# Optimization experiments

Measured on AMD Instinct MI355X. Metric: run time of the kernel, lower is better.

## Reference

```python
import jax, jax.numpy as jnp
import numpy as np

N, F, H, E, G, C = 100000, 128, 128, 640000, 512, 6
EPS = 1e-5


def setup_inputs() -> dict:
    key = jax.random.key(0)
    ks = jax.random.split(key, 20)
    def w(k, shape, fan_in):
        return jax.random.normal(k, shape, jnp.float32) * (1.0 / np.sqrt(fan_in))
    return {
        "x": jax.random.normal(ks[0], (N, F), jnp.float32),
        "edge_index": jax.random.randint(ks[1], (2, E), 0, N),
        "batch": jnp.sort(jax.random.randint(ks[2], (N,), 0, G)),
        "num_graphs": G,
        # SAGEConv1: lin_l (aggregated, with bias) + lin_r (root, no bias)
        "W1l": w(ks[3], (F, H), F), "b1l": jnp.zeros((H,), jnp.float32), "W1r": w(ks[4], (F, H), F),
        # SAGEConv2
        "W2l": w(ks[5], (H, H), H), "b2l": jnp.zeros((H,), jnp.float32), "W2r": w(ks[6], (H, H), H),
        # cluster heads
        "Wc1": w(ks[7], (H, H), H), "bc1": jnp.zeros((H,), jnp.float32),
        "Wc2": w(ks[8], (H, 2), H), "bc2": jnp.zeros((2,), jnp.float32),
        # classifier
        "Wl1": w(ks[9], (H, H), H), "bl1": jnp.zeros((H,), jnp.float32),
        "Wl2": w(ks[10], (H, C), H), "bl2": jnp.zeros((C,), jnp.float32),
    }


def _sage(x, src, dst, Wl, bl, Wr):
    # PyG SAGEConv: mean-aggregate messages x[src] at dst, then lin_l(agg) + lin_r(x)
    n = x.shape[0]
    s = jax.ops.segment_sum(x[src], dst, num_segments=n)
    cnt = jax.ops.segment_sum(jnp.ones((src.shape[0],), x.dtype), dst, num_segments=n)
    agg = s / jnp.maximum(cnt, 1.0)[:, None]
    return agg @ Wl + bl + x @ Wr


def reference(x, edge_index, batch, num_graphs,
              W1l, b1l, W1r, W2l, b2l, W2r,
              Wc1, bc1, Wc2, bc2, Wl1, bl1, Wl2, bl2):
    src, dst = edge_index[0], edge_index[1]
    h = jax.nn.relu(_sage(x, src, dst, W1l, b1l, W1r))
    h = jax.nn.relu(_sage(h, src, dst, W2l, b2l, W2r))
    # 2-way soft cluster assignment per node
    a = jax.nn.softmax(jnp.tanh(h @ Wc1 + bc1) @ Wc2 + bc2, axis=1)  # [N,2]
    g = num_graphs
    # group_features[g] = a_g^T h_g  -> per-node outer product, segment-summed by graph
    gf = jax.ops.segment_sum(a[:, :, None] * h[:, None, :], batch, num_segments=g)  # [G,2,H]
    pos = gf[:, 0, :]  # positive-cluster embedding per graph
    # new_adj[g] = a_g^T A_g a_g ; only within-graph edges appear in the per-graph adj block
    same = (batch[src] == batch[dst]).astype(h.dtype)
    contrib = same[:, None, None] * (a[src][:, :, None] * a[dst][:, None, :])  # [E,2,2]
    new_adj = jax.ops.segment_sum(contrib, batch[src], num_segments=g)  # [G,2,2]
    # F.normalize(p=1, dim=1, eps=1e-5): row-wise L1 with clamped denominator
    l1 = jnp.sum(jnp.abs(new_adj), axis=2, keepdims=True)
    norm_adj = new_adj / jnp.maximum(l1, EPS)
    diag = jnp.diagonal(norm_adj, axis1=1, axis2=2)  # [G,2]
    penalty = jnp.mean(jnp.mean((diag - 1.0) ** 2, axis=1))  # mse vs ones(2), averaged over graphs
    # NOTE: original (faithfully reproduced) takes the mean over ALL nodes, same for every graph
    graph_emb = jnp.broadcast_to(jnp.mean(h, axis=0, keepdims=True), (g, h.shape[1]))
    z = jax.nn.relu(pos @ Wl1 + bl1)  # dropout off (eval mode)
    logits = z @ Wl2 + bl2
    return (jax.nn.log_softmax(logits, axis=-1), pos, graph_emb, penalty)
```

## Files before the change

kernel.cpp:

```cpp
#include <hip/hip_runtime.h>

#define NN 100000
#define NE 640000
#define HD 128
#define NG 512
#define NC 6
#define EPSV 1e-5f
#define OCT 12500

typedef __bf16 bf16_t;
typedef bf16_t bf16x8 __attribute__((ext_vector_type(8)));
typedef float f32x4 __attribute__((ext_vector_type(4)));

__device__ __forceinline__ float b2f(unsigned int u16) {
    return __builtin_bit_cast(float, u16 << 16);
}
__device__ __forceinline__ unsigned short f2b(float f) {
    unsigned int u = __builtin_bit_cast(unsigned int, f);
    unsigned int r = (u + 0x7fffu + ((u >> 16) & 1u)) >> 16;
    return (unsigned short)r;
}

__global__ __launch_bounds__(256) void k_zero(uint4* __restrict__ p, int n16) {
    int i = blockIdx.x * 256 + threadIdx.x;
    if (i < n16) p[i] = (uint4){0u, 0u, 0u, 0u};
}

__global__ __launch_bounds__(256) void k_prep(
    const float* __restrict__ x, unsigned short* __restrict__ xb,
    const float* __restrict__ Wa, const float* __restrict__ Wb,
    const float* __restrict__ Wc, const float* __restrict__ Wd,
    const float* __restrict__ We, unsigned short* __restrict__ Wt,
    const int* __restrict__ dst, int* __restrict__ cnt)
{
    int bid = blockIdx.x;
    if (bid < 960) {
        int oct = bid & 7;
        int widx = bid >> 3;
        int lo = oct * OCT, hi = lo + OCT;
        for (int e = widx * 256 + threadIdx.x; e < NE; e += 120 * 256) {
            int d = dst[e];
            if (d >= lo && d < hi) atomicAdd(&cnt[d], 1);
        }
    } else if (bid < 7210) {
        int i = (bid - 960) * 256 + threadIdx.x;
        float4 v0 = reinterpret_cast<const float4*>(x)[i * 2];
        float4 v1 = reinterpret_cast<const float4*>(x)[i * 2 + 1];
        unsigned short u[8] = {f2b(v0.x), f2b(v0.y), f2b(v0.z), f2b(v0.w),
                               f2b(v1.x), f2b(v1.y), f2b(v1.z), f2b(v1.w)};
        reinterpret_cast<uint4*>(xb)[i] = *reinterpret_cast<uint4*>(u);
    } else {
        int i = (bid - 7210) * 256 + threadIdx.x;
        int w = i >> 14, r = i & 16383;
        int k = r >> 7, n = r & 127;
        const float* W = (w == 0) ? Wa : (w == 1) ? Wb : (w == 2) ? Wc : (w == 3) ? Wd : We;
        Wt[w * 16384 + n * HD + k] = f2b(W[k * HD + n]);
    }
}

__global__ void k_scan1(const int* __restrict__ cnt, int* __restrict__ excl,
                        int* __restrict__ bsum, int n) {
    __shared__ int sh[256];
    int i = blockIdx.x * 256 + threadIdx.x;
    int v = (i < n) ? cnt[i] : 0;
    sh[threadIdx.x] = v;
    __syncthreads();
    for (int off = 1; off < 256; off <<= 1) {
        int t = (threadIdx.x >= off) ? sh[threadIdx.x - off] : 0;
        __syncthreads();
        sh[threadIdx.x] += t;
        __syncthreads();
    }
    if (i < n) excl[i] = sh[threadIdx.x] - v;
    if (threadIdx.x == 255) bsum[blockIdx.x] = sh[255];
}

__global__ void k_scan2(int* bsum, int nb) {
    __shared__ int sh[512];
    int t = threadIdx.x;
    sh[t] = (t < nb) ? bsum[t] : 0;
    __syncthreads();
    for (int off = 1; off < 512; off <<= 1) {
        int v = (t >= off) ? sh[t - off] : 0;
        __syncthreads();
        sh[t] += v;
        __syncthreads();
    }
    if (t < nb) bsum[t] = sh[t];
}

__global__ void k_scan3(const int* __restrict__ excl, const int* __restrict__ bsum,
                        int* __restrict__ row_off, int n) {
    int i = blockIdx.x * 256 + threadIdx.x;
    if (i < n) row_off[i] = excl[i] + (blockIdx.x ? bsum[blockIdx.x - 1] : 0);
    if (i == 0) row_off[n] = NE;
}

__global__ __launch_bounds__(256) void k_fill(const int* __restrict__ src,
                                              const int* __restrict__ dst,
                                              const int* __restrict__ row_off,
                                              int* __restrict__ cnt,
                                              int* __restrict__ csr) {
    int q = blockIdx.x;
    int oct = q & 7;
    int widx = q >> 3;
    int lo = oct * OCT, hi = lo + OCT;
    for (int e = widx * 256 + threadIdx.x; e < NE; e += 120 * 256) {
        int d = dst[e];
        if (d >= lo && d < hi) {
            int p = atomicSub(&cnt[d], 1);
            csr[row_off[d] + p - 1] = src[e];
        }
    }
}

__global__ __launch_bounds__(256) void k_sage(
    const unsigned short* __restrict__ X,
    const int* __restrict__ row_off, const int* __restrict__ csr,
    const unsigned short* __restrict__ Wlt, const unsigned short* __restrict__ Wrt,
    const float* __restrict__ bias, unsigned short* __restrict__ out, int M)
{
    __shared__ uint4 wlds[4096];
    const int wid = threadIdx.x >> 6;
    const int lane = threadIdx.x & 63;
    const int lrow = lane & 15;
    const int lkg = lane >> 4;
    const int r0 = blockIdx.x * 64 + wid * 16;

    const uint4* gl = reinterpret_cast<const uint4*>(Wlt);
    const uint4* gr = reinterpret_cast<const uint4*>(Wrt);
    for (int i = threadIdx.x; i < 2048; i += 256) {
        int di = i ^ ((i >> 4) & 7);
        wlds[di] = gl[i];
        wlds[2048 + di] = gr[i];
    }

    int row = r0 + lrow;
    row = row < M ? row : M - 1;
    int beg = row_off[row], end = row_off[row + 1];

    float accg[4][8];
#pragma unroll
    for (int ks = 0; ks < 4; ++ks)
#pragma unroll
        for (int j = 0; j < 8; ++j) accg[ks][j] = 0.f;

    const unsigned short* Xk = X + lkg * 8;
    for (int j = beg; j < end; j += 2) {
        int s0 = csr[j];
        const unsigned short* p0 = Xk + (size_t)s0 * HD;
        uint4 w0 = *reinterpret_cast<const uint4*>(p0);
        uint4 w1 = *reinterpret_cast<const uint4*>(p0 + 32);
        uint4 w2 = *reinterpret_cast<const uint4*>(p0 + 64);
        uint4 w3 = *reinterpret_cast<const uint4*>(p0 + 96);
        bool ok1 = (j + 1) < end;
        int s1 = csr[ok1 ? j + 1 : j];
        const unsigned short* p1 = Xk + (size_t)s1 * HD;
        uint4 y0, y1, y2, y3;
        if (ok1) {
            y0 = *reinterpret_cast<const uint4*>(p1);
            y1 = *reinterpret_cast<const uint4*>(p1 + 32);
            y2 = *reinterpret_cast<const uint4*>(p1 + 64);
            y3 = *reinterpret_cast<const uint4*>(p1 + 96);
        }
        accg[0][0] += b2f(w0.x & 0xffffu); accg[0][1] += b2f(w0.x >> 16);
        accg[0][2] += b2f(w0.y & 0xffffu); accg[0][3] += b2f(w0.y >> 16);
        accg[0][4] += b2f(w0.z & 0xffffu); accg[0][5] += b2f(w0.z >> 16);
        accg[0][6] += b2f(w0.w & 0xffffu); accg[0][7] += b2f(w0.w >> 16);
        accg[1][0] += b2f(w1.x & 0xffffu); accg[1][1] += b2f(w1.x >> 16);
        accg[1][2] += b2f(w1.y & 0xffffu); accg[1][3] += b2f(w1.y >> 16);
        accg[1][4] += b2f(w1.z & 0xffffu); accg[1][5] += b2f(w1.z >> 16);
        accg[1][6] += b2f(w1.w & 0xffffu); accg[1][7] += b2f(w1.w >> 16);
        accg[2][0] += b2f(w2.x & 0xffffu); accg[2][1] += b2f(w2.x >> 16);
        accg[2][2] += b2f(w2.y & 0xffffu); accg[2][3] += b2f(w2.y >> 16);
        accg[2][4] += b2f(w2.z & 0xffffu); accg[2][5] += b2f(w2.z >> 16);
        accg[2][6] += b2f(w2.w & 0xffffu); accg[2][7] += b2f(w2.w >> 16);
        accg[3][0] += b2f(w3.x & 0xffffu); accg[3][1] += b2f(w3.x >> 16);
        accg[3][2] += b2f(w3.y & 0xffffu); accg[3][3] += b2f(w3.y >> 16);
        accg[3][4] += b2f(w3.z & 0xffffu); accg[3][5] += b2f(w3.z >> 16);
        accg[3][6] += b2f(w3.w & 0xffffu); accg[3][7] += b2f(w3.w >> 16);
        if (ok1) {
            accg[0][0] += b2f(y0.x & 0xffffu); accg[0][1] += b2f(y0.x >> 16);
            accg[0][2] += b2f(y0.y & 0xffffu); accg[0][3] += b2f(y0.y >> 16);
            accg[0][4] += b2f(y0.z & 0xffffu); accg[0][5] += b2f(y0.z >> 16);
            accg[0][6] += b2f(y0.w & 0xffffu); accg[0][7] += b2f(y0.w >> 16);
            accg[1][0] += b2f(y1.x & 0xffffu); accg[1][1] += b2f(y1.x >> 16);
            accg[1][2] += b2f(y1.y & 0xffffu); accg[1][3] += b2f(y1.y >> 16);
            accg[1][4] += b2f(y1.z & 0xffffu); accg[1][5] += b2f(y1.z >> 16);
            accg[1][6] += b2f(y1.w & 0xffffu); accg[1][7] += b2f(y1.w >> 16);
            accg[2][0] += b2f(y2.x & 0xffffu); accg[2][1] += b2f(y2.x >> 16);
            accg[2][2] += b2f(y2.y & 0xffffu); accg[2][3] += b2f(y2.y >> 16);
            accg[2][4] += b2f(y2.z & 0xffffu); accg[2][5] += b2f(y2.z >> 16);
            accg[2][6] += b2f(y2.w & 0xffffu); accg[2][7] += b2f(y2.w >> 16);
            accg[3][0] += b2f(y3.x & 0xffffu); accg[3][1] += b2f(y3.x >> 16);
            accg[3][2] += b2f(y3.y & 0xffffu); accg[3][3] += b2f(y3.y >> 16);
            accg[3][4] += b2f(y3.z & 0xffffu); accg[3][5] += b2f(y3.z >> 16);
            accg[3][6] += b2f(y3.w & 0xffffu); accg[3][7] += b2f(y3.w >> 16);
        }
    }

    float inv = 1.f / fmaxf((float)(end - beg), 1.f);
    bf16x8 a1[4], a2f[4];
#pragma unroll
    for (int ks = 0; ks < 4; ++ks) {
        unsigned short u[8];
#pragma unroll
        for (int j = 0; j < 8; ++j) u[j] = f2b(accg[ks][j] * inv);
        a1[ks] = *reinterpret_cast<bf16x8*>(u);
    }
    const unsigned short* p2 = X + (size_t)row * HD + lkg * 8;
#pragma unroll
    for (int ks = 0; ks < 4; ++ks)
        a2f[ks] = *reinterpret_cast<const bf16x8*>(p2 + ks * 32);

    f32x4 acc[8];
#pragma unroll
    for (int t = 0; t < 8; ++t) {
        float b = bias[t * 16 + lrow];
        acc[t] = (f32x4){b, b, b, b};
    }

    __syncthreads();

    const char* ldsb = (const char*)wlds;
#pragma unroll
    for (int ks = 0; ks < 4; ++ks) {
#pragma unroll
        for (int t = 0; t < 8; ++t) {
            int off = (lrow * 256 + lkg * 16 + t * 4096 + ks * 64) ^ ((lrow & 7) << 4);
            bf16x8 bl = *reinterpret_cast<const bf16x8*>(ldsb + off);
            bf16x8 br = *reinterpret_cast<const bf16x8*>(ldsb + 32768 + off);
            acc[t] = __builtin_amdgcn_mfma_f32_16x16x32_bf16(a1[ks], bl, acc[t], 0, 0, 0);
            acc[t] = __builtin_amdgcn_mfma_f32_16x16x32_bf16(a2f[ks], br, acc[t], 0, 0, 0);
        }
    }

#pragma unroll
    for (int t = 0; t < 8; ++t)
#pragma unroll
        for (int r = 0; r < 4; ++r) {
            int orow = r0 + lkg * 4 + r;
            if (orow < M)
                out[(size_t)orow * HD + t * 16 + lrow] = f2b(fmaxf(acc[t][r], 0.f));
        }
}

__global__ __launch_bounds__(256) void mfma_attn(
    const unsigned short* __restrict__ A1, const unsigned short* __restrict__ W1t,
    const float* __restrict__ bias, const float* __restrict__ Wc2,
    const float* __restrict__ bc2, float* __restrict__ a2, int M)
{
    __shared__ uint4 wlds[2048];
    const int wid = threadIdx.x >> 6;
    const int lane = threadIdx.x & 63;
    const int lrow = lane & 15;
    const int lkg = lane >> 4;
    const int r0 = blockIdx.x * 128 + wid * 32;

    bf16x8 a[2][4];
#pragma unroll
    for (int g = 0; g < 2; ++g) {
        int row = r0 + g * 16 + lrow;
        row = row < M ? row : M - 1;
        const unsigned short* p = A1 + (size_t)row * HD + lkg * 8;
#pragma unroll
        for (int ks = 0; ks < 4; ++ks)
            a[g][ks] = *reinterpret_cast<const bf16x8*>(p + ks * 32);
    }

    f32x4 acc[2][8];
#pragma unroll
    for (int t = 0; t < 8; ++t) {
        float b = bias[t * 16 + lrow];
        acc[0][t] = (f32x4){b, b, b, b};
        acc[1][t] = (f32x4){b, b, b, b};
    }

    const uint4* g4 = reinterpret_cast<const uint4*>(W1t);
    for (int i = threadIdx.x; i < 2048; i += 256) {
        int di = i ^ ((i >> 4) & 7);
        wlds[di] = g4[i];
    }
    __syncthreads();

    const char* ldsb = (const char*)wlds;
#pragma unroll
    for (int ks = 0; ks < 4; ++ks) {
#pragma unroll
        for (int t = 0; t < 8; ++t) {
            int off = (lrow * 256 + lkg * 16 + t * 4096 + ks * 64) ^ ((lrow & 7) << 4);
            bf16x8 b = *reinterpret_cast<const bf16x8*>(ldsb + off);
            acc[0][t] = __builtin_amdgcn_mfma_f32_16x16x32_bf16(a[0][ks], b, acc[0][t], 0, 0, 0);
            acc[1][t] = __builtin_amdgcn_mfma_f32_16x16x32_bf16(a[1][ks], b, acc[1][t], 0, 0, 0);
        }
    }

    float p0[2][4] = {{0.f, 0.f, 0.f, 0.f}, {0.f, 0.f, 0.f, 0.f}};
    float p1[2][4] = {{0.f, 0.f, 0.f, 0.f}, {0.f, 0.f, 0.f, 0.f}};
#pragma unroll
    for (int t = 0; t < 8; ++t) {
        float2 wv = reinterpret_cast<const float2*>(Wc2)[t * 16 + lrow];
#pragma unroll
        for (int g = 0; g < 2; ++g)
#pragma unroll
            for (int r = 0; r < 4; ++r) {
                float tv = tanhf(acc[g][t][r]);
                p0[g][r] = fmaf(tv, wv.x, p0[g][r]);
                p1[g][r] = fmaf(tv, wv.y, p1[g][r]);
            }
    }
#pragma unroll
    for (int off = 1; off < 16; off <<= 1) {
#pragma unroll
        for (int g = 0; g < 2; ++g)
#pragma unroll
            for (int r = 0; r < 4; ++r) {
                p0[g][r] += __shfl_xor(p0[g][r], off, 64);
                p1[g][r] += __shfl_xor(p1[g][r], off, 64);
            }
    }
    if (lrow == 0) {
        float B0 = bc2[0], B1 = bc2[1];
#pragma unroll
        for (int g = 0; g < 2; ++g)
#pragma unroll
            for (int r = 0; r < 4; ++r) {
                int row = r0 + g * 16 + lkg * 4 + r;
                if (row < M) {
                    float u0 = p0[g][r] + B0, u1 = p1[g][r] + B1;
                    float m = fmaxf(u0, u1);
                    float e0 = expf(u0 - m), e1 = expf(u1 - m);
                    float inv = 1.f / (e0 + e1);
                    reinterpret_cast<float2*>(a2)[row] = (float2){e0 * inv, e1 * inv};
                }
            }
    }
}

__global__ __launch_bounds__(1024) void k_posadj(const unsigned short* __restrict__ h,
                                                 const float* __restrict__ a2,
                                                 const int* __restrict__ batch,
                                                 const int* __restrict__ src,
                                                 const int* __restrict__ dst,
                                                 float* __restrict__ pos_out,
                                                 float* __restrict__ csum,
                                                 float* __restrict__ adj) {
    __shared__ float4 sh[16][64];
    __shared__ float shadj[NG * 4];
    int bid = blockIdx.x;
    if (bid < NG) {
        int g = bid;
        int lo = 0, hi = NN;
        while (lo < hi) { int m = (lo + hi) >> 1; if (batch[m] < g) lo = m + 1; else hi = m; }
        int beg = lo;
        hi = NN;
        while (lo < hi) { int m = (lo + hi) >> 1; if (batch[m] < g + 1) lo = m + 1; else hi = m; }
        int end = lo;
        int grp = threadIdx.x >> 6;
        int lane = threadIdx.x & 63;
        float4 acc = {0.f, 0.f, 0.f, 0.f};
        for (int i = beg + grp * 2; i < end; i += 32) {
            int i1 = i + 1;
            bool ok1 = i1 < end;
            float a0 = a2[i * 2];
            unsigned int v0 = *reinterpret_cast<const unsigned int*>(h + (size_t)i * HD + lane * 2);
            float a1 = ok1 ? a2[i1 * 2] : 0.f;
            unsigned int v1 = ok1 ? *reinterpret_cast<const unsigned int*>(h + (size_t)i1 * HD + lane * 2) : 0u;
            float f0 = b2f(v0 & 0xffffu), f1 = b2f(v0 >> 16);
            float g0 = b2f(v1 & 0xffffu), g1 = b2f(v1 >> 16);
            acc.x = fmaf(a0, f0, fmaf(a1, g0, acc.x));
            acc.y = fmaf(a0, f1, fmaf(a1, g1, acc.y));
            acc.z += f0 + g0;
            acc.w += f1 + g1;
        }
        sh[grp][lane] = acc;
        __syncthreads();
        if (threadIdx.x < 64) {
            float4 s = sh[0][lane];
#pragma unroll
            for (int k = 1; k < 16; ++k) {
                float4 t = sh[k][lane];
                s.x += t.x; s.y += t.y; s.z += t.z; s.w += t.w;
            }
            reinterpret_cast<float2*>(pos_out)[g * 64 + lane] = (float2){s.x, s.y};
            atomicAdd(&csum[lane * 2], s.z);
            atomicAdd(&csum[lane * 2 + 1], s.w);
        }
    } else {
        for (int i = threadIdx.x; i < NG * 4; i += 1024) shadj[i] = 0.f;
        __syncthreads();
        for (int e = (bid - NG) * 1024 + threadIdx.x; e < NE; e += 120 * 1024) {
            int s = src[e], d = dst[e];
            int bs = batch[s], bd = batch[d];
            if (bs != bd) continue;
            float a0s = a2[2 * s], a1s = a2[2 * s + 1];
            float a0d = a2[2 * d], a1d = a2[2 * d + 1];
            float* A = shadj + bs * 4;
            atomicAdd(A + 0, a0s * a0d);
            atomicAdd(A + 1, a0s * a1d);
            atomicAdd(A + 2, a1s * a0d);
            atomicAdd(A + 3, a1s * a1d);
        }
        __syncthreads();
        for (int i = threadIdx.x; i < NG * 4; i += 1024) {
            float v = shadj[i];
            if (v != 0.f) atomicAdd(&adj[i], v);
        }
    }
}

__global__ __launch_bounds__(512) void k_tail(const float* __restrict__ csum,
                                              float* __restrict__ gemb_out,
                                              const float* __restrict__ adj,
                                              float* __restrict__ pen) {
    int bid = blockIdx.x;
    if (bid < 128) {
        int i = bid * 512 + threadIdx.x;
        gemb_out[i] = csum[i & 127] * (1.f / (float)NN);
    } else {
        __shared__ float sh[512];
        int g = threadIdx.x;
        float x0 = adj[g * 4], x1 = adj[g * 4 + 1], x2 = adj[g * 4 + 2], x3 = adj[g * 4 + 3];
        float l0 = fabsf(x0) + fabsf(x1);
        float l1 = fabsf(x2) + fabsf(x3);
        float d0 = x0 / fmaxf(l0, EPSV);
        float d1 = x3 / fmaxf(l1, EPSV);
        sh[g] = 0.5f * ((d0 - 1.f) * (d0 - 1.f) + (d1 - 1.f) * (d1 - 1.f));
        __syncthreads();
        for (int off = 256; off >= 1; off >>= 1) {
            if (g < off) sh[g] += sh[g + off];
            __syncthreads();
        }
        if (g == 0) pen[0] = sh[0] * (1.f / (float)NG);
    }
}

__global__ __launch_bounds__(256) void gemm_head(
    const float* __restrict__ A, const float* __restrict__ W,
    const float* __restrict__ bias, float* __restrict__ out, int M)
{
    const int tid = threadIdx.x;
    const int w = __builtin_amdgcn_readfirstlane(tid >> 6);
    const int lane = tid & 63;
    const int r0 = blockIdx.x * 32 + w * 8;
    if (r0 >= M) return;
    const int c0 = lane, c1 = lane + 64;
    float acc0[8], acc1[8];
    const float b0 = bias[c0], b1 = bias[c1];
#pragma unroll
    for (int r = 0; r < 8; ++r) { acc0[r] = b0; acc1[r] = b1; }
    const float* Ap = A + (size_t)r0 * HD;
    for (int k4 = 0; k4 < HD / 4; ++k4) {
        float4 a[8];
#pragma unroll
        for (int r = 0; r < 8; ++r)
            a[r] = *reinterpret_cast<const float4*>(Ap + r * HD + k4 * 4);
#pragma unroll
        for (int j = 0; j < 4; ++j) {
            const int k = k4 * 4 + j;
            const float w0 = W[k * HD + c0];
            const float w1 = W[k * HD + c1];
#pragma unroll
            for (int r = 0; r < 8; ++r) {
                const float av = (j == 0) ? a[r].x : (j == 1) ? a[r].y
                               : (j == 2) ? a[r].z : a[r].w;
                acc0[r] = fmaf(av, w0, acc0[r]);
                acc1[r] = fmaf(av, w1, acc1[r]);
            }
        }
    }
#pragma unroll
    for (int r = 0; r < 8; ++r) {
        out[(size_t)(r0 + r) * HD + c0] = fmaxf(acc0[r], 0.f);
        out[(size_t)(r0 + r) * HD + c1] = fmaxf(acc1[r], 0.f);
    }
}

__global__ void k_head(const float* __restrict__ z, const float* __restrict__ Wl2,
                       const float* __restrict__ bl2, float* __restrict__ out0) {
    int g = blockIdx.x * blockDim.x + threadIdx.x;
    if (g >= NG) return;
    float l[NC];
#pragma unroll
    for (int c = 0; c < NC; ++c) l[c] = bl2[c];
    for (int k = 0; k < HD; ++k) {
        float zv = z[(size_t)g * HD + k];
#pragma unroll
        for (int c = 0; c < NC; ++c) l[c] = fmaf(zv, Wl2[k * NC + c], l[c]);
    }
    float m = l[0];
#pragma unroll
    for (int c = 1; c < NC; ++c) m = fmaxf(m, l[c]);
    float sum = 0.f;
#pragma unroll
    for (int c = 0; c < NC; ++c) sum += expf(l[c] - m);
    float lse = m + logf(sum);
#pragma unroll
    for (int c = 0; c < NC; ++c) out0[g * NC + c] = l[c] - lse;
}

extern "C" void kernel_launch(void* const* d_in, const int* in_sizes, int n_in,
                              void* d_out, int out_size, void* d_ws, size_t ws_size,
                              hipStream_t stream) {
    const float* x   = (const float*)d_in[0];
    const int*   ei  = (const int*)d_in[1];
    const int*   src = ei;
    const int*   dst = ei + NE;
    const int*   batch = (const int*)d_in[2];
    const float* W1l = (const float*)d_in[4];
    const float* b1l = (const float*)d_in[5];
    const float* W1r = (const float*)d_in[6];
    const float* W2l = (const float*)d_in[7];
    const float* b2l = (const float*)d_in[8];
    const float* W2r = (const float*)d_in[9];
    const float* Wc1 = (const float*)d_in[10];
    const float* bc1 = (const float*)d_in[11];
    const float* Wc2 = (const float*)d_in[12];
    const float* bc2 = (const float*)d_in[13];
    const float* Wl1 = (const float*)d_in[14];
    const float* bl1 = (const float*)d_in[15];
    const float* Wl2 = (const float*)d_in[16];
    const float* bl2 = (const float*)d_in[17];

    char* ws = (char*)d_ws;
    const size_t BB = (size_t)NN * HD * 2;
    unsigned short* xb   = (unsigned short*)(ws);
    unsigned short* bufB = (unsigned short*)(ws + BB);
    size_t O = 2 * BB;
    int*   cnt     = (int*)(ws + O);
    float* adj     = (float*)(ws + O + 400000);
    float* csum    = (float*)(ws + O + 408192);
    int*   row_off = (int*)(ws + O + 408704);
    int*   excl    = (int*)(ws + O + 808768);
    int*   bsum    = (int*)(ws + O + 1208768);
    int*   csr     = (int*)(ws + O + 1212864);
    float* a2      = (float*)(ws + O + 3772864);
    float* zbuf    = (float*)(ws + O + 4572864);
    unsigned short* w1lt = (unsigned short*)(ws + O + 4835008);
    unsigned short* w1rt = w1lt + 16384;
    unsigned short* w2lt = w1rt + 16384;
    unsigned short* w2rt = w2lt + 16384;
    unsigned short* wc1t = w2rt + 16384;

    float* out0 = (float*)d_out;
    float* pos  = out0 + NG * NC;
    float* gemb = pos + NG * HD;
    float* pen  = gemb + NG * HD;

    k_zero<<<100, 256, 0, stream>>>((uint4*)(ws + O), 25544);
    k_prep<<<7530, 256, 0, stream>>>(x, xb, W1l, W1r, W2l, W2r, Wc1, w1lt, dst, cnt);
    k_scan1<<<391, 256, 0, stream>>>(cnt, excl, bsum, NN);
    k_scan2<<<1, 512, 0, stream>>>(bsum, 391);
    k_scan3<<<391, 256, 0, stream>>>(excl, bsum, row_off, NN);
    k_fill<<<960, 256, 0, stream>>>(src, dst, row_off, cnt, csr);

    const int SAGE_GRID = (NN + 63) / 64;
    k_sage<<<SAGE_GRID, 256, 0, stream>>>(xb, row_off, csr, w1lt, w1rt, b1l, bufB, NN);
    k_sage<<<SAGE_GRID, 256, 0, stream>>>(bufB, row_off, csr, w2lt, w2rt, b2l, xb, NN);
    mfma_attn<<<(NN + 127) / 128, 256, 0, stream>>>(xb, wc1t, bc1, Wc2, bc2, a2, NN);
    k_posadj<<<NG + 120, 1024, 0, stream>>>(xb, a2, batch, src, dst, pos, csum, adj);
    k_tail<<<129, 512, 0, stream>>>(csum, gemb, adj, pen);
    gemm_head<<<NG / 32, 256, 0, stream>>>(pos, Wl1, bl1, zbuf, NG);
    k_head<<<2, 256, 0, stream>>>(zbuf, Wl2, bl2, out0);
}
```

Measured before the change: 289.2 us.

## Pre-swizzle weights into MFMA fragment order and load directly from global

The weight prep kernel now writes bf16 weights in MFMA B-fragment order, so each lane's 8-element operand is one contiguous 16-byte chunk. The SAGE and attention kernels drop their LDS weight staging and __syncthreads, and load fragments straight from global memory (L1/L2 cached). Loops are reordered to finish each 16-column output tile before starting the next, which cuts live accumulator registers. This removes LDS usage and the block-wide barrier, which may raise occupancy, but every wave now issues its own global weight loads, with more latency exposed right before the MFMAs.

```diff
diff --git a/kernel.cpp b/kernel.cpp
--- a/kernel.cpp
+++ b/kernel.cpp
@@ -51,10 +51,13 @@
         reinterpret_cast<uint4*>(xb)[i] = *reinterpret_cast<uint4*>(u);
     } else {
         int i = (bid - 7210) * 256 + threadIdx.x;
-        int w = i >> 14, r = i & 16383;
-        int k = r >> 7, n = r & 127;
+        int w = i >> 14, f = i & 16383;
+        int fu = f >> 3, e = f & 7;
+        int g2 = fu >> 6, ln = fu & 63;
+        int n = (g2 >> 2) * 16 + (ln & 15);
+        int k = ((g2 & 3) * 4 + (ln >> 4)) * 8 + e;
         const float* W = (w == 0) ? Wa : (w == 1) ? Wb : (w == 2) ? Wc : (w == 3) ? Wd : We;
-        Wt[w * 16384 + n * HD + k] = f2b(W[k * HD + n]);
+        Wt[w * 16384 + f] = f2b(W[k * HD + n]);
     }
 }
 
@@ -117,23 +120,14 @@
 __global__ __launch_bounds__(256) void k_sage(
     const unsigned short* __restrict__ X,
     const int* __restrict__ row_off, const int* __restrict__ csr,
-    const unsigned short* __restrict__ Wlt, const unsigned short* __restrict__ Wrt,
+    const unsigned short* __restrict__ Wlf, const unsigned short* __restrict__ Wrf,
     const float* __restrict__ bias, unsigned short* __restrict__ out, int M)
 {
-    __shared__ uint4 wlds[4096];
     const int wid = threadIdx.x >> 6;
     const int lane = threadIdx.x & 63;
     const int lrow = lane & 15;
     const int lkg = lane >> 4;
     const int r0 = blockIdx.x * 64 + wid * 16;
-
-    const uint4* gl = reinterpret_cast<const uint4*>(Wlt);
-    const uint4* gr = reinterpret_cast<const uint4*>(Wrt);
-    for (int i = threadIdx.x; i < 2048; i += 256) {
-        int di = i ^ ((i >> 4) & 7);
-        wlds[di] = gl[i];
-        wlds[2048 + di] = gr[i];
-    }
 
     int row = r0 + lrow;
     row = row < M ? row : M - 1;
@@ -213,44 +207,31 @@
     for (int ks = 0; ks < 4; ++ks)
         a2f[ks] = *reinterpret_cast<const bf16x8*>(p2 + ks * 32);
 
-    f32x4 acc[8];
 #pragma unroll
     for (int t = 0; t < 8; ++t) {
         float b = bias[t * 16 + lrow];
-        acc[t] = (f32x4){b, b, b, b};
-    }
-
-    __syncthreads();
-
-    const char* ldsb = (const char*)wlds;
-#pragma unroll
-    for (int ks = 0; ks < 4; ++ks) {
-#pragma unroll
-        for (int t = 0; t < 8; ++t) {
-            int off = (lrow * 256 + lkg * 16 + t * 4096 + ks * 64) ^ ((lrow & 7) << 4);
-            bf16x8 bl = *reinterpret_cast<const bf16x8*>(ldsb + off);
-            bf16x8 br = *reinterpret_cast<const bf16x8*>(ldsb + 32768 + off);
-            acc[t] = __builtin_amdgcn_mfma_f32_16x16x32_bf16(a1[ks], bl, acc[t], 0, 0, 0);
-            acc[t] = __builtin_amdgcn_mfma_f32_16x16x32_bf16(a2f[ks], br, acc[t], 0, 0, 0);
-        }
-    }
-
-#pragma unroll
-    for (int t = 0; t < 8; ++t)
+        f32x4 acc = (f32x4){b, b, b, b};
+#pragma unroll
+        for (int ks = 0; ks < 4; ++ks) {
+            bf16x8 bl = *reinterpret_cast<const bf16x8*>(Wlf + ((t * 4 + ks) * 64 + lane) * 8);
+            bf16x8 br = *reinterpret_cast<const bf16x8*>(Wrf + ((t * 4 + ks) * 64 + lane) * 8);
+            acc = __builtin_amdgcn_mfma_f32_16x16x32_bf16(a1[ks], bl, acc, 0, 0, 0);
+            acc = __builtin_amdgcn_mfma_f32_16x16x32_bf16(a2f[ks], br, acc, 0, 0, 0);
+        }
 #pragma unroll
         for (int r = 0; r < 4; ++r) {
             int orow = r0 + lkg * 4 + r;
             if (orow < M)
-                out[(size_t)orow * HD + t * 16 + lrow] = f2b(fmaxf(acc[t][r], 0.f));
-        }
+                out[(size_t)orow * HD + t * 16 + lrow] = f2b(fmaxf(acc[r], 0.f));
+        }
+    }
 }
 
 __global__ __launch_bounds__(256) void mfma_attn(
-    const unsigned short* __restrict__ A1, const unsigned short* __restrict__ W1t,
+    const unsigned short* __restrict__ A1, const unsigned short* __restrict__ Wf,
     const float* __restrict__ bias, const float* __restrict__ Wc2,
     const float* __restrict__ bc2, float* __restrict__ a2, int M)
 {
-    __shared__ uint4 wlds[2048];
     const int wid = threadIdx.x >> 6;
     const int lane = threadIdx.x & 63;
     const int lrow = lane & 15;
@@ -268,46 +249,30 @@
             a[g][ks] = *reinterpret_cast<const bf16x8*>(p + ks * 32);
     }
 
-    f32x4 acc[2][8];
+    float p0[2][4] = {{0.f, 0.f, 0.f, 0.f}, {0.f, 0.f, 0.f, 0.f}};
+    float p1[2][4] = {{0.f, 0.f, 0.f, 0.f}, {0.f, 0.f, 0.f, 0.f}};
+
 #pragma unroll
     for (int t = 0; t < 8; ++t) {
         float b = bias[t * 16 + lrow];
-        acc[0][t] = (f32x4){b, b, b, b};
-        acc[1][t] = (f32x4){b, b, b, b};
-    }
-
-    const uint4* g4 = reinterpret_cast<const uint4*>(W1t);
-    for (int i = threadIdx.x; i < 2048; i += 256) {
-        int di = i ^ ((i >> 4) & 7);
-        wlds[di] = g4[i];
-    }
-    __syncthreads();
-
-    const char* ldsb = (const char*)wlds;
-#pragma unroll
-    for (int ks = 0; ks < 4; ++ks) {
-#pragma unroll
-        for (int t = 0; t < 8; ++t) {
-            int off = (lrow * 256 + lkg * 16 + t * 4096 + ks * 64) ^ ((lrow & 7) << 4);
-            bf16x8 b = *reinterpret_cast<const bf16x8*>(ldsb + off);
-            acc[0][t] = __builtin_amdgcn_mfma_f32_16x16x32_bf16(a[0][ks], b, acc[0][t], 0, 0, 0);
-            acc[1][t] = __builtin_amdgcn_mfma_f32_16x16x32_bf16(a[1][ks], b, acc[1][t], 0, 0, 0);
-        }
-    }
-
-    float p0[2][4] = {{0.f, 0.f, 0.f, 0.f}, {0.f, 0.f, 0.f, 0.f}};
-    float p1[2][4] = {{0.f, 0.f, 0.f, 0.f}, {0.f, 0.f, 0.f, 0.f}};
-#pragma unroll
-    for (int t = 0; t < 8; ++t) {
+        f32x4 acc0 = (f32x4){b, b, b, b};
+        f32x4 acc1 = acc0;
+#pragma unroll
+        for (int ks = 0; ks < 4; ++ks) {
+            bf16x8 bw = *reinterpret_cast<const bf16x8*>(Wf + ((t * 4 + ks) * 64 + lane) * 8);
+            acc0 = __builtin_amdgcn_mfma_f32_16x16x32_bf16(a[0][ks], bw, acc0, 0, 0, 0);
+            acc1 = __builtin_amdgcn_mfma_f32_16x16x32_bf16(a[1][ks], bw, acc1, 0, 0, 0);
+        }
         float2 wv = reinterpret_cast<const float2*>(Wc2)[t * 16 + lrow];
 #pragma unroll
-        for (int g = 0; g < 2; ++g)
-#pragma unroll
-            for (int r = 0; r < 4; ++r) {
-                float tv = tanhf(acc[g][t][r]);
-                p0[g][r] = fmaf(tv, wv.x, p0[g][r]);
-                p1[g][r] = fmaf(tv, wv.y, p1[g][r]);
-            }
+        for (int r = 0; r < 4; ++r) {
+            float tv0 = tanhf(acc0[r]);
+            float tv1 = tanhf(acc1[r]);
+            p0[0][r] = fmaf(tv0, wv.x, p0[0][r]);
+            p1[0][r] = fmaf(tv0, wv.y, p1[0][r]);
+            p0[1][r] = fmaf(tv1, wv.x, p0[1][r]);
+            p1[1][r] = fmaf(tv1, wv.y, p1[1][r]);
+        }
     }
 #pragma unroll
     for (int off = 1; off < 16; off <<= 1) {
```

After: 280.2 us. -3.1%, faster.
